# Kernel optimization log

Hardware: AMD Instinct MI355X
Metric: run time of the kernel (lower is better)

Reference implementation:

```python
import jax, jax.numpy as jnp
import numpy as np

REG_WEIGHT = 1e-4
N_LAYERS = 3


def setup_inputs() -> dict:
    key = jax.random.key(0)
    ks = jax.random.split(key, 7)
    n_users, n_items, d = 100000, 50000, 64
    E, B = 1600000, 4096
    return {
        "user_table": jax.random.normal(ks[0], (n_users, d), dtype=jnp.float32) * 0.01,
        "item_table": jax.random.normal(ks[1], (n_items, d), dtype=jnp.float32) * 0.01,
        "edge_u": jax.random.randint(ks[2], (E,), 0, n_users, dtype=jnp.int32),
        "edge_i": jax.random.randint(ks[3], (E,), 0, n_items, dtype=jnp.int32),
        "users": jax.random.randint(ks[4], (B,), 0, n_users, dtype=jnp.int32),
        "pos_items": jax.random.randint(ks[5], (B,), 0, n_items, dtype=jnp.int32),
        "neg_items": jax.random.randint(ks[6], (B,), 0, n_items, dtype=jnp.int32),
    }


def _lightgcn_embeddings(user_table, item_table, edge_u, edge_i):
    n_users, n_items = user_table.shape[0], item_table.shape[0]
    N = n_users + n_items
    E = edge_u.shape[0]
    ones = jnp.ones((E,), dtype=user_table.dtype)
    # symmetric normalization D^{-1/2} A D^{-1/2} on the bipartite graph
    deg_u = jax.ops.segment_sum(ones, edge_u, num_segments=n_users)
    deg_i = jax.ops.segment_sum(ones, edge_i, num_segments=n_items)
    w = jax.lax.rsqrt(jnp.maximum(deg_u[edge_u] * deg_i[edge_i], 1.0))
    # symmetric edge list over the stacked [users; items] node set
    rows = jnp.concatenate([edge_u, edge_i + n_users])
    cols = jnp.concatenate([edge_i + n_users, edge_u])
    vals = jnp.concatenate([w, w])[:, None]

    x = jnp.concatenate([user_table, item_table], axis=0)  # [N, d]
    acc = x
    for _ in range(N_LAYERS):
        x = jax.ops.segment_sum(x[cols] * vals, rows, num_segments=N)
        acc = acc + x
    final = acc / jnp.asarray(N_LAYERS + 1, dtype=x.dtype)
    return final[:n_users], final[n_users:]


def reference(user_table, item_table, edge_u, edge_i, users, pos_items, neg_items):
    user_emb_all, item_emb_all = _lightgcn_embeddings(user_table, item_table, edge_u, edge_i)
    u_emb = user_emb_all[users]
    pos_i_emb = item_emb_all[pos_items]
    neg_i_emb = item_emb_all[neg_items]
    pos_scores = jnp.sum(u_emb * pos_i_emb, axis=-1)
    neg_scores = jnp.sum(u_emb * neg_i_emb, axis=-1)
    # L2 regularization on the layer-0 (table) embeddings
    u0 = user_table[users]
    p0 = item_table[pos_items]
    n0 = item_table[neg_items]
    reg_loss = REG_WEIGHT * (jnp.sum(u0 * u0) + jnp.sum(p0 * p0) + jnp.sum(n0 * n0))
    reg_loss = reg_loss / users.shape[0]
    return pos_scores, neg_scores, reg_loss
```

## Files before the change

### kernel.cpp

```cpp
#include <hip/hip_runtime.h>
#include <hip/hip_fp16.h>

#define THREADS 256
#define BIN_C 4096
#define NBMAX 400
#define CAP 4608
#define SH_U 8
#define SH_I 7
#define CPAD 16

__global__ void bin_kernel(const int* __restrict__ eu, const int* __restrict__ ei,
                           int* __restrict__ bcnt_u, int* __restrict__ bcnt_i,
                           int* __restrict__ binu, int* __restrict__ bini,
                           int E, int nbu, int nbi) {
    __shared__ int hist_u[NBMAX], hist_i[NBMAX];
    __shared__ int base_u[NBMAX], base_i[NBMAX];
    int tid = threadIdx.x;
    int e0 = blockIdx.x * BIN_C;
    if (e0 >= E) return;
    int cnt = min(BIN_C, E - e0);

    for (int b = tid; b < NBMAX; b += THREADS) { hist_u[b] = 0; hist_i[b] = 0; }
    __syncthreads();

    int u[16], v[16];
    #pragma unroll
    for (int j = 0; j < 16; ++j) {
        int k = tid + j * THREADS;
        if (k < cnt) { u[j] = eu[e0 + k]; v[j] = ei[e0 + k]; }
        else         { u[j] = -1; v[j] = -1; }
    }
    #pragma unroll
    for (int j = 0; j < 16; ++j) {
        if (u[j] >= 0) {
            atomicAdd(&hist_u[u[j] >> SH_U], 1);
            atomicAdd(&hist_i[v[j] >> SH_I], 1);
        }
    }
    __syncthreads();
    for (int b = tid; b < NBMAX; b += THREADS) {
        int cu = hist_u[b], ci = hist_i[b];
        base_u[b] = (cu > 0 && b < nbu) ? atomicAdd(&bcnt_u[(size_t)b * CPAD], cu) : 0;
        base_i[b] = (ci > 0 && b < nbi) ? atomicAdd(&bcnt_i[(size_t)b * CPAD], ci) : 0;
        hist_u[b] = 0; hist_i[b] = 0;
    }
    __syncthreads();
    #pragma unroll
    for (int j = 0; j < 16; ++j) {
        if (u[j] >= 0) {
            int bu = u[j] >> SH_U;
            int pu = base_u[bu] + atomicAdd(&hist_u[bu], 1);
            if (pu < CAP) binu[(size_t)bu * CAP + pu] = ((u[j] & 255) << 16) | v[j];
            int bi = v[j] >> SH_I;
            int pi = base_i[bi] + atomicAdd(&hist_i[bi], 1);
            if (pi < CAP) bini[(size_t)bi * CAP + pi] = ((v[j] & 127) << 17) | u[j];
        }
    }
}

__global__ void bucket_off(const int* __restrict__ bcnt, int* __restrict__ bo,
                           int* __restrict__ cursor, int nb, int pad) {
    int idx = blockIdx.x * blockDim.x + threadIdx.x;
    int lane = threadIdx.x & 63;
    int d = 0;
    if (idx < nb) d = min(bcnt[(size_t)idx * CPAD], CAP) + pad;
    int s = d;
    #pragma unroll
    for (int ofs = 1; ofs < 64; ofs <<= 1) {
        int t = __shfl_up(s, ofs);
        if (lane >= ofs) s += t;
    }
    int total = __shfl(s, 63);
    int base = 0;
    if (lane == 63) base = atomicAdd(cursor, total);
    base = __shfl(base, 63);
    if (idx < nb) bo[idx] = base + s - d;
}

__global__ void place(const int* __restrict__ bcnt_u, const int* __restrict__ bcnt_i,
                      const int* __restrict__ bo_u, const int* __restrict__ bo_i,
                      const int* __restrict__ binu, const int* __restrict__ bini,
                      int* __restrict__ offu, int* __restrict__ offi,
                      int* __restrict__ du, int* __restrict__ di,
                      float* __restrict__ rsdu, float* __restrict__ rsdi,
                      int* __restrict__ entu, int* __restrict__ enti,
                      int nbu, int nU, int nI) {
    __shared__ int stash[CAP];
    __shared__ int cnt[THREADS];
    __shared__ int wcur[THREADS];
    __shared__ int scan[THREADS];
    int b = blockIdx.x;
    bool isU = (b < nbu);
    const int* bin; int base_node, nn, count, bob, n_tot;
    int *off, *deg, *ent; float* rsd;
    if (isU) {
        bin = binu + (size_t)b * CAP;
        base_node = b << SH_U; n_tot = nU; nn = min(256, nU - base_node);
        count = min(bcnt_u[(size_t)b * CPAD], CAP); bob = bo_u[b];
        off = offu; deg = du; rsd = rsdu; ent = entu;
    } else {
        int b2 = b - nbu;
        bin = bini + (size_t)b2 * CAP;
        base_node = b2 << SH_I; n_tot = nI; nn = min(128, nI - base_node);
        count = min(bcnt_i[(size_t)b2 * CPAD], CAP); bob = bo_i[b2];
        off = offi; deg = di; rsd = rsdi; ent = enti;
    }
    int tid = threadIdx.x;
    cnt[tid] = 0;
    __syncthreads();
    for (int k = tid; k < count; k += THREADS) {
        int p = bin[k];
        stash[k] = p;
        int lo = isU ? (p >> 16) : (p >> 17);
        atomicAdd(&cnt[lo], 1);
    }
    __syncthreads();
    int c = cnt[tid];
    int seg = (c + 15) & ~15;
    scan[tid] = seg;
    __syncthreads();
    #pragma unroll
    for (int ofs = 1; ofs < THREADS; ofs <<= 1) {
        int t = (tid >= ofs) ? scan[tid - ofs] : 0;
        __syncthreads();
        scan[tid] += t;
        __syncthreads();
    }
    int excl = scan[tid] - seg;
    wcur[tid] = excl;
    if (tid < nn) {
        off[base_node + tid] = bob + excl;
        deg[base_node + tid] = c;
        rsd[base_node + tid] = rsqrtf(fmaxf((float)c, 1.0f));
    }
    __syncthreads();
    int lomask = isU ? 0xFFFF : 0x1FFFF;
    for (int k = tid; k < count; k += THREADS) {
        int p = stash[k];
        int lo = isU ? (p >> 16) : (p >> 17);
        int sl = atomicAdd(&wcur[lo], 1);
        ent[bob + sl] = p & lomask;
    }
}

__global__ void conv16(const float* __restrict__ src, __half* __restrict__ dst, int n4) {
    int stride = gridDim.x * blockDim.x;
    for (int i = blockIdx.x * blockDim.x + threadIdx.x; i < n4; i += stride) {
        float4 v = *reinterpret_cast<const float4*>(src + (size_t)i * 4);
        __half2 h0 = __float22half2_rn(make_float2(v.x, v.y));
        __half2 h1 = __float22half2_rn(make_float2(v.z, v.w));
        uint2 st;
        st.x = *reinterpret_cast<unsigned*>(&h0);
        st.y = *reinterpret_cast<unsigned*>(&h1);
        *reinterpret_cast<uint2*>(dst + (size_t)i * 4) = st;
    }
}

__global__ void prop16(const __half* __restrict__ x,
                       const int* __restrict__ offu, const int* __restrict__ offi,
                       const int* __restrict__ du, const int* __restrict__ di,
                       const float* __restrict__ rsdu, const float* __restrict__ rsdi,
                       const int* __restrict__ entu, const int* __restrict__ enti,
                       __half* __restrict__ y, int nU, int N) {
    int node = blockIdx.x * (THREADS >> 3) + (threadIdx.x >> 3);
    int lane = threadIdx.x & 7;
    if (node >= N) return;
    const int* ent; const __half* src; const float* rsdn;
    int beg, dg; float rs;
    if (node < nU) {
        beg = offu[node]; dg = du[node]; rs = rsdu[node];
        ent = entu; src = x + ((size_t)nU << 6); rsdn = rsdi;
    } else {
        int i = node - nU;
        beg = offi[i]; dg = di[i]; rs = rsdi[i];
        ent = enti; src = x; rsdn = rsdu;
    }
    float a0=0,a1=0,a2=0,a3=0,a4=0,a5=0,a6=0,a7=0;
    for (int k0 = 0; k0 < dg; k0 += 8) {
        int me = (k0 + lane < dg) ? ent[beg + k0 + lane] : 0;
        #pragma unroll
        for (int j = 0; j < 8; ++j) {
            if (k0 + j < dg) {
                int nbr = __shfl(me, j, 8);
                float w = rsdn[nbr];
                uint4 r = *reinterpret_cast<const uint4*>(src + ((size_t)nbr << 6) + (lane << 3));
                __half2 h0 = *reinterpret_cast<__half2*>(&r.x);
                __half2 h1 = *reinterpret_cast<__half2*>(&r.y);
                __half2 h2 = *reinterpret_cast<__half2*>(&r.z);
                __half2 h3 = *reinterpret_cast<__half2*>(&r.w);
                float2 f0 = __half22float2(h0), f1 = __half22float2(h1);
                float2 f2 = __half22float2(h2), f3 = __half22float2(h3);
                a0 += w * f0.x; a1 += w * f0.y; a2 += w * f1.x; a3 += w * f1.y;
                a4 += w * f2.x; a5 += w * f2.y; a6 += w * f3.x; a7 += w * f3.y;
            }
        }
    }
    __half2 o0 = __float22half2_rn(make_float2(a0 * rs, a1 * rs));
    __half2 o1 = __float22half2_rn(make_float2(a2 * rs, a3 * rs));
    __half2 o2 = __float22half2_rn(make_float2(a4 * rs, a5 * rs));
    __half2 o3 = __float22half2_rn(make_float2(a6 * rs, a7 * rs));
    uint4 st;
    st.x = *reinterpret_cast<unsigned*>(&o0);
    st.y = *reinterpret_cast<unsigned*>(&o1);
    st.z = *reinterpret_cast<unsigned*>(&o2);
    st.w = *reinterpret_cast<unsigned*>(&o3);
    *reinterpret_cast<uint4*>(y + ((size_t)node << 6) + (lane << 3)) = st;
}

__global__ void sel_init(const float* __restrict__ ut, const float* __restrict__ it,
                         const int* __restrict__ users, const int* __restrict__ pos,
                         const int* __restrict__ neg, float* __restrict__ sel, int B) {
    int r = blockIdx.x * (THREADS >> 4) + (threadIdx.x >> 4);
    int t = threadIdx.x & 15;
    if (r >= 3 * B) return;
    int which = r / B, b = r - which * B;
    const float* base; int idx;
    if (which == 0)      { base = ut; idx = users[b]; }
    else if (which == 1) { base = it; idx = pos[b]; }
    else                 { base = it; idx = neg[b]; }
    float4 v = *reinterpret_cast<const float4*>(base + ((size_t)idx << 6) + t * 4);
    *reinterpret_cast<float4*>(sel + ((size_t)r << 6) + t * 4) = v;
}

__global__ void sel_acc16(const __half* __restrict__ x,
                          const int* __restrict__ users, const int* __restrict__ pos,
                          const int* __restrict__ neg, float* __restrict__ sel, int B, int nU) {
    int r = blockIdx.x * (THREADS >> 3) + (threadIdx.x >> 3);
    int lane = threadIdx.x & 7;
    if (r >= 3 * B) return;
    int which = r / B, b = r - which * B;
    size_t row;
    if (which == 0)      row = (size_t)users[b];
    else if (which == 1) row = (size_t)nU + pos[b];
    else                 row = (size_t)nU + neg[b];
    uint4 rv = *reinterpret_cast<const uint4*>(x + (row << 6) + (lane << 3));
    __half2 h0 = *reinterpret_cast<__half2*>(&rv.x);
    __half2 h1 = *reinterpret_cast<__half2*>(&rv.y);
    __half2 h2 = *reinterpret_cast<__half2*>(&rv.z);
    __half2 h3 = *reinterpret_cast<__half2*>(&rv.w);
    float2 f0 = __half22float2(h0), f1 = __half22float2(h1);
    float2 f2 = __half22float2(h2), f3 = __half22float2(h3);
    float* s = sel + ((size_t)r << 6) + (lane << 3);
    float4 d0 = *reinterpret_cast<float4*>(s);
    float4 d1 = *reinterpret_cast<float4*>(s + 4);
    d0.x += f0.x; d0.y += f0.y; d0.z += f1.x; d0.w += f1.y;
    d1.x += f2.x; d1.y += f2.y; d1.z += f3.x; d1.w += f3.y;
    *reinterpret_cast<float4*>(s) = d0;
    *reinterpret_cast<float4*>(s + 4) = d1;
}

__global__ void score(const float* __restrict__ sel, float* __restrict__ out, int B) {
    int b = blockIdx.x * (THREADS >> 6) + (threadIdx.x >> 6);
    int lane = threadIdx.x & 63;
    if (b >= B) return;
    float u = sel[((size_t)b << 6) + lane];
    float p = sel[((size_t)(B + b) << 6) + lane];
    float n = sel[((size_t)(2 * B + b) << 6) + lane];
    float ps = u * p, ns = u * n;
    for (int ofs = 32; ofs; ofs >>= 1) {
        ps += __shfl_down(ps, ofs);
        ns += __shfl_down(ns, ofs);
    }
    if (lane == 0) {
        out[b]     = ps * (1.0f / 16.0f);
        out[B + b] = ns * (1.0f / 16.0f);
    }
}

__global__ void regk(const float* __restrict__ ut, const float* __restrict__ it,
                     const int* __restrict__ users, const int* __restrict__ pos,
                     const int* __restrict__ neg,
                     float* __restrict__ out_reg, int B, float scale) {
    int total = 3 * B * 64;
    float s = 0.f;
    int stride = gridDim.x * blockDim.x;
    for (int idx = blockIdx.x * blockDim.x + threadIdx.x; idx < total; idx += stride) {
        int r = idx >> 6, d = idx & 63;
        int which = r / B, b = r - which * B;
        float v;
        if (which == 0)      v = ut[((size_t)users[b] << 6) + d];
        else if (which == 1) v = it[((size_t)pos[b] << 6) + d];
        else                 v = it[((size_t)neg[b] << 6) + d];
        s += v * v;
    }
    for (int ofs = 32; ofs; ofs >>= 1) s += __shfl_down(s, ofs);
    __shared__ float sh[4];
    int lane = threadIdx.x & 63, wid = threadIdx.x >> 6;
    if (lane == 0) sh[wid] = s;
    __syncthreads();
    if (threadIdx.x == 0) {
        float tot = 0.f;
        for (int i = 0; i < (int)(blockDim.x >> 6); ++i) tot += sh[i];
        atomicAdd(out_reg, tot * scale);
    }
}

extern "C" void kernel_launch(void* const* d_in, const int* in_sizes, int n_in,
                              void* d_out, int out_size, void* d_ws, size_t ws_size,
                              hipStream_t stream) {
    const float* ut   = (const float*)d_in[0];
    const float* it   = (const float*)d_in[1];
    const int* eu     = (const int*)d_in[2];
    const int* ei     = (const int*)d_in[3];
    const int* users  = (const int*)d_in[4];
    const int* pos    = (const int*)d_in[5];
    const int* neg    = (const int*)d_in[6];
    int nU = in_sizes[0] / 64;
    int nI = in_sizes[1] / 64;
    int E  = in_sizes[2];
    int B  = in_sizes[4];
    int N  = nU + nI;
    float* out = (float*)d_out;

    int nbu = (nU + 255) >> SH_U;
    int nbi = (nI + 127) >> SH_I;

    char* ws = (char*)d_ws;
    size_t cursor = 0;
    auto alloc = [&](size_t bytes) -> void* {
        cursor = (cursor + 255) & ~(size_t)255;
        void* p = ws + cursor;
        cursor += bytes;
        return p;
    };
    int*   bcnt_u = (int*)alloc((size_t)nbu * CPAD * 4);
    int*   bcnt_i = (int*)alloc((size_t)nbi * CPAD * 4);
    int*   curs   = (int*)alloc(2 * 4);
    size_t zero_span = cursor;
    int*   bo_u = (int*)alloc((size_t)nbu * 4);
    int*   bo_i = (int*)alloc((size_t)nbi * 4);
    int*   binu = (int*)alloc((size_t)nbu * CAP * 4);
    int*   bini = (int*)alloc((size_t)nbi * CAP * 4);
    int*   offu = (int*)alloc((size_t)nU * 4);
    int*   offi = (int*)alloc((size_t)nI * 4);
    int*   du   = (int*)alloc((size_t)nU * 4);
    int*   di   = (int*)alloc((size_t)nI * 4);
    float* rsdu = (float*)alloc((size_t)nU * 4);
    float* rsdi = (float*)alloc((size_t)nI * 4);
    int*   entu = (int*)alloc(((size_t)E + (size_t)nbu * 256 * 16) * 4);
    int*   enti = (int*)alloc(((size_t)E + (size_t)nbi * 128 * 16) * 4);
    __half* xA  = (__half*)alloc((size_t)N * 64 * 2);
    __half* xB  = (__half*)alloc((size_t)N * 64 * 2);
    float* sel  = (float*)alloc((size_t)3 * B * 64 * 4);

    hipMemsetAsync(d_ws, 0, zero_span, stream);
    hipMemsetAsync(out + 2 * B, 0, sizeof(float), stream);

    conv16<<<2048, THREADS, 0, stream>>>(ut, xA, nU * 16);
    conv16<<<2048, THREADS, 0, stream>>>(it, xA + ((size_t)nU << 6), nI * 16);

    int nchunks = (E + BIN_C - 1) / BIN_C;
    bin_kernel<<<nchunks, THREADS, 0, stream>>>(eu, ei, bcnt_u, bcnt_i, binu, bini, E, nbu, nbi);
    bucket_off<<<(nbu + THREADS - 1) / THREADS, THREADS, 0, stream>>>(bcnt_u, bo_u, curs, nbu, 256 * 16);
    bucket_off<<<(nbi + THREADS - 1) / THREADS, THREADS, 0, stream>>>(bcnt_i, bo_i, curs + 1, nbi, 128 * 16);
    place<<<nbu + nbi, THREADS, 0, stream>>>(bcnt_u, bcnt_i, bo_u, bo_i, binu, bini,
                                             offu, offi, du, di, rsdu, rsdi, entu, enti,
                                             nbu, nU, nI);

    int gridSel16 = (3 * B * 8 + THREADS - 1) / THREADS;
    sel_init<<<(3 * B + 15) / 16, THREADS, 0, stream>>>(ut, it, users, pos, neg, sel, B);

    int gridProp = (N * 8 + THREADS - 1) / THREADS;
    prop16<<<gridProp, THREADS, 0, stream>>>(xA, offu, offi, du, di, rsdu, rsdi, entu, enti, xB, nU, N);
    sel_acc16<<<gridSel16, THREADS, 0, stream>>>(xB, users, pos, neg, sel, B, nU);
    prop16<<<gridProp, THREADS, 0, stream>>>(xB, offu, offi, du, di, rsdu, rsdi, entu, enti, xA, nU, N);
    sel_acc16<<<gridSel16, THREADS, 0, stream>>>(xA, users, pos, neg, sel, B, nU);
    prop16<<<gridProp, THREADS, 0, stream>>>(xA, offu, offi, du, di, rsdu, rsdi, entu, enti, xB, nU, N);
    sel_acc16<<<gridSel16, THREADS, 0, stream>>>(xB, users, pos, neg, sel, B, nU);

    score<<<(B + 3) / 4, THREADS, 0, stream>>>(sel, out, B);
    regk<<<256, THREADS, 0, stream>>>(ut, it, users, pos, neg, out + 2 * B, B, 1e-4f / (float)B);
}
```

Measured before the change: 311.7 us.

## Compute final propagation layer only for selected batch nodes

The last propagation layer no longer runs over all N nodes. It is replaced by a kernel that aggregates neighbours only for the 3B selected user and item rows and adds the result straight into the selection accumulator. This avoids a full-graph SpMM pass and the write of the full layer-3 embedding array. The trade-off is somewhat irregular per-row work, since selected nodes are processed in a batch with uneven degrees.

```diff
diff --git a/kernel.cpp b/kernel.cpp
--- a/kernel.cpp
+++ b/kernel.cpp
@@ -207,6 +207,58 @@
     *reinterpret_cast<uint4*>(y + ((size_t)node << 6) + (lane << 3)) = st;
 }
 
+__global__ void prop_sel(const __half* __restrict__ x,
+                         const int* __restrict__ users, const int* __restrict__ pos,
+                         const int* __restrict__ neg,
+                         const int* __restrict__ offu, const int* __restrict__ offi,
+                         const int* __restrict__ du, const int* __restrict__ di,
+                         const float* __restrict__ rsdu, const float* __restrict__ rsdi,
+                         const int* __restrict__ entu, const int* __restrict__ enti,
+                         float* __restrict__ sel, int B, int nU) {
+    int r = blockIdx.x * (THREADS >> 3) + (threadIdx.x >> 3);
+    int lane = threadIdx.x & 7;
+    if (r >= 3 * B) return;
+    int which = r / B, b = r - which * B;
+    const int* ent; const __half* src; const float* rsdn;
+    int beg, dg; float rs;
+    if (which == 0) {
+        int u = users[b];
+        beg = offu[u]; dg = du[u]; rs = rsdu[u];
+        ent = entu; src = x + ((size_t)nU << 6); rsdn = rsdi;
+    } else {
+        int i = (which == 1) ? pos[b] : neg[b];
+        beg = offi[i]; dg = di[i]; rs = rsdi[i];
+        ent = enti; src = x; rsdn = rsdu;
+    }
+    float a0=0,a1=0,a2=0,a3=0,a4=0,a5=0,a6=0,a7=0;
+    for (int k0 = 0; k0 < dg; k0 += 8) {
+        int me = (k0 + lane < dg) ? ent[beg + k0 + lane] : 0;
+        #pragma unroll
+        for (int j = 0; j < 8; ++j) {
+            if (k0 + j < dg) {
+                int nbr = __shfl(me, j, 8);
+                float w = rsdn[nbr];
+                uint4 rv = *reinterpret_cast<const uint4*>(src + ((size_t)nbr << 6) + (lane << 3));
+                __half2 h0 = *reinterpret_cast<__half2*>(&rv.x);
+                __half2 h1 = *reinterpret_cast<__half2*>(&rv.y);
+                __half2 h2 = *reinterpret_cast<__half2*>(&rv.z);
+                __half2 h3 = *reinterpret_cast<__half2*>(&rv.w);
+                float2 f0 = __half22float2(h0), f1 = __half22float2(h1);
+                float2 f2 = __half22float2(h2), f3 = __half22float2(h3);
+                a0 += w * f0.x; a1 += w * f0.y; a2 += w * f1.x; a3 += w * f1.y;
+                a4 += w * f2.x; a5 += w * f2.y; a6 += w * f3.x; a7 += w * f3.y;
+            }
+        }
+    }
+    float* s = sel + ((size_t)r << 6) + (lane << 3);
+    float4 d0 = *reinterpret_cast<float4*>(s);
+    float4 d1 = *reinterpret_cast<float4*>(s + 4);
+    d0.x += rs * a0; d0.y += rs * a1; d0.z += rs * a2; d0.w += rs * a3;
+    d1.x += rs * a4; d1.y += rs * a5; d1.z += rs * a6; d1.w += rs * a7;
+    *reinterpret_cast<float4*>(s) = d0;
+    *reinterpret_cast<float4*>(s + 4) = d1;
+}
+
 __global__ void sel_init(const float* __restrict__ ut, const float* __restrict__ it,
                          const int* __restrict__ users, const int* __restrict__ pos,
                          const int* __restrict__ neg, float* __restrict__ sel, int B) {
@@ -365,8 +417,8 @@
     sel_acc16<<<gridSel16, THREADS, 0, stream>>>(xB, users, pos, neg, sel, B, nU);
     prop16<<<gridProp, THREADS, 0, stream>>>(xB, offu, offi, du, di, rsdu, rsdi, entu, enti, xA, nU, N);
     sel_acc16<<<gridSel16, THREADS, 0, stream>>>(xA, users, pos, neg, sel, B, nU);
-    prop16<<<gridProp, THREADS, 0, stream>>>(xA, offu, offi, du, di, rsdu, rsdi, entu, enti, xB, nU, N);
-    sel_acc16<<<gridSel16, THREADS, 0, stream>>>(xB, users, pos, neg, sel, B, nU);
+    prop_sel<<<gridSel16, THREADS, 0, stream>>>(xA, users, pos, neg, offu, offi, du, di,
+                                                rsdu, rsdi, entu, enti, sel, B, nU);
 
     score<<<(B + 3) / 4, THREADS, 0, stream>>>(sel, out, B);
     regk<<<256, THREADS, 0, stream>>>(ut, it, users, pos, neg, out + 2 * B, B, 1e-4f / (float)B);
```

Measured after the change: 268.4 us. 1.16x faster.
